# Kernel tuning notes

Measured on AMD Instinct MI355X. Metric: run time of the kernel, lower is better.

Reference implementation:

```python
import jax, jax.numpy as jnp
import numpy as np

B, S, DIN, DOUT = 4, 2048, 4096, 4096

def setup_inputs() -> dict:
    key = jax.random.key(0)
    k1, k2, k3, k4 = jax.random.split(key, 4)
    x = jax.random.normal(k1, (B, S, DIN), dtype=jnp.float32)
    # symmetric int8 weight values in [-127, 127]
    quantized_weight = jax.random.randint(k2, (DOUT, DIN), -127, 128, dtype=jnp.int32).astype(jnp.int8)
    weight_scale = jax.random.uniform(k3, (), dtype=jnp.float32) * 0.01 + 1e-4
    bias = jax.random.normal(k4, (DOUT,), dtype=jnp.float32)
    return {"x": x, "quantized_weight": quantized_weight, "weight_scale": weight_scale, "bias": bias}

def reference(x, quantized_weight, weight_scale, bias) -> jnp.ndarray:
    # dequantize_tensor: (q.float() - 0) * scale
    weight_fp32 = quantized_weight.astype(jnp.float32) * weight_scale  # [DOUT, DIN]
    # nn.functional.linear: x @ W^T + b
    return jnp.einsum('bsi,oi->bso', x, weight_fp32) + bias
```

## Files before the change

### kernel.cpp

```cpp
#include <hip/hip_runtime.h>
#include <stdint.h>
#include <stddef.h>

constexpr int MDIM = 8192;
constexpr int NDIM = 4096;
constexpr int KDIM = 4096;

using f32x4 = __attribute__((ext_vector_type(4))) float;
using s16x4 = __attribute__((ext_vector_type(4))) short;
using i32x4 = __attribute__((ext_vector_type(4))) int;

__device__ __forceinline__ short f32_to_bf16_rn(float f) {
  union { float f; uint32_t u; } v; v.f = f;
  uint32_t r = (v.u + 0x7FFFu + ((v.u >> 16) & 1u)) >> 16;
  return (short)(uint16_t)r;
}

__global__ void __launch_bounds__(256) quant_x_kernel(const float* __restrict__ in,
                                                      signed char* __restrict__ out,
                                                      float* __restrict__ sx) {
  const int row = blockIdx.x;
  const int t   = threadIdx.x;
  const float* rp = in + (size_t)row * KDIM;
  f32x4 v[4];
  float m = 0.0f;
#pragma unroll
  for (int j = 0; j < 4; ++j) {
    v[j] = *(const f32x4*)(rp + t * 16 + j * 4);
#pragma unroll
    for (int e = 0; e < 4; ++e) m = fmaxf(m, __builtin_fabsf(v[j][e]));
  }
#pragma unroll
  for (int off = 32; off > 0; off >>= 1) m = fmaxf(m, __shfl_xor(m, off, 64));
  __shared__ float wmax[4];
  const int wv = t >> 6, ln = t & 63;
  if (ln == 0) wmax[wv] = m;
  __syncthreads();
  m = fmaxf(fmaxf(wmax[0], wmax[1]), fmaxf(wmax[2], wmax[3]));
  const float inv = (m > 0.0f) ? (127.0f / m) : 0.0f;
  if (t == 0) sx[row] = m * (1.0f / 127.0f);
  i32x4 o;
#pragma unroll
  for (int j = 0; j < 4; ++j) {
    int b[4];
#pragma unroll
    for (int e = 0; e < 4; ++e) {
      int q = (int)rintf(v[j][e] * inv);
      q = q < -127 ? -127 : (q > 127 ? 127 : q);
      b[e] = q & 255;
    }
    o[j] = b[0] | (b[1] << 8) | (b[2] << 16) | (b[3] << 24);
  }
  *(i32x4*)(out + (size_t)row * KDIM + t * 16) = o;
}

__global__ void __launch_bounds__(256) quant_w_kernel(const int* __restrict__ in,
                                                      signed char* __restrict__ out, int n16) {
  int i = blockIdx.x * 256 + threadIdx.x;
  const int stride = gridDim.x * 256;
  for (; i < n16; i += stride) {
    const i32x4* p = (const i32x4*)(in + (size_t)i * 16);
    i32x4 o;
#pragma unroll
    for (int j = 0; j < 4; ++j) {
      i32x4 a = p[j];
      o[j] = (a[0] & 255) | ((a[1] & 255) << 8) | ((a[2] & 255) << 16) | ((a[3] & 255) << 24);
    }
    *(i32x4*)(out + (size_t)i * 16) = o;
  }
}


#define BAR asm volatile("s_barrier" ::: "memory")
#define WAITVM6 asm volatile("s_waitcnt vmcnt(6)" ::: "memory")
#define WAITVM0 asm volatile("s_waitcnt vmcnt(0)" ::: "memory")

#define GLL(src, dst) __builtin_amdgcn_global_load_lds(                     \
    (const __attribute__((address_space(1))) void*)(src),                   \
    (__attribute__((address_space(3))) void*)(dst), 16, 0, 0)

#define STAGE(grow, ldsmat, ks, tau) do {                                   \
  const int buf_ = (tau) & 1;                                               \
  GLL((grow) + (size_t)r0 * 4096 + (size_t)(tau) * 128 + (ks) * 64 + cb,    \
      lds + (ldsmat) + buf_ * 32768 + (ks) * 16384 + t * 16);               \
  GLL((grow) + (size_t)r1 * 4096 + (size_t)(tau) * 128 + (ks) * 64 + cb,    \
      lds + (ldsmat) + buf_ * 32768 + (ks) * 16384 + 8192 + t * 16);        \
} while (0)

#define LDA(cur, ks, i) (*(const i32x4*)(lds + (cur) * 32768 + (ks) * 16384 \
    + (wm * 8 + (i)) * 1024 + laneoff))
#define LDB(cur, ks, j) (*(const i32x4*)(lds + 65536 + (cur) * 32768        \
    + (ks) * 16384 + (wn * 4 + (j)) * 1024 + laneoff))

#define READ_B(cur, ks) do {                                                \
  _Pragma("unroll") for (int j = 0; j < 4; ++j) bf[j] = LDB(cur, ks, j);    \
} while (0)
#define READ_A(cur, ks, ibase) do {                                         \
  _Pragma("unroll") for (int i = 0; i < 4; ++i) af[i] = LDA(cur, ks, (ibase) + i); \
} while (0)

#define MFMA16(ibase) do {                                                  \
  __builtin_amdgcn_s_setprio(1);                                            \
  _Pragma("unroll") for (int i = 0; i < 4; ++i)                             \
  _Pragma("unroll") for (int j = 0; j < 4; ++j)                             \
    acc[(ibase) + i][j] = __builtin_amdgcn_mfma_i32_16x16x64_i8(            \
        af[i], bf[j], acc[(ibase) + i][j], 0, 0, 0);                        \
  __builtin_amdgcn_s_setprio(0);                                            \
} while (0)

#define KTILE(t_, cur, nstage, endvm) do {                                  \
                                                   \
  READ_B(cur, 0); READ_A(cur, 0, 0);                                        \
  if ((nstage) >= 1) STAGE(Arow, 0, 1, (t_) + 1);        \
  BAR; MFMA16(0); BAR;                                                      \
                                        \
  READ_A(cur, 0, 4);                                                        \
  if ((nstage) == 4) STAGE(Brow, 65536, 0, (t_) + 2);    \
  BAR; MFMA16(4); BAR;                                                      \
                                                   \
  READ_B(cur, 1); READ_A(cur, 1, 0);                                        \
  if ((nstage) == 4) STAGE(Arow, 0, 0, (t_) + 2);        \
  BAR; MFMA16(0); BAR;                                                      \
                                                   \
  READ_A(cur, 1, 4);                                                        \
  if ((nstage) == 4) STAGE(Brow, 65536, 1, (t_) + 2);    \
  BAR; MFMA16(4);                                                           \
  if ((endvm) == 6) { WAITVM6; } else if ((endvm) == 0) { WAITVM0; }        \
  BAR;                                                                      \
} while (0)

__global__ void __launch_bounds__(512, 2) gemm_i8_8ph(
    const signed char* __restrict__ A, const signed char* __restrict__ Bw,
    const float* __restrict__ sx, const float* __restrict__ scale_p,
    const float* __restrict__ bias, float* __restrict__ out) {
  __shared__ __align__(16) char lds[131072];

  const int t      = threadIdx.x;
  const int lane   = t & 63;
  const int wave   = t >> 6;
  const int wm     = wave >> 2;
  const int wn     = wave & 3;
  const int lane15 = lane & 15;
  const int lh     = lane >> 4;

  const int laneoff = (lane15 * 64 + lh * 16) ^ ((lane15 & 8) << 2);

  const int ax = ((t >> 5) & 1) << 5;
  const int a0 = (t * 16) ^ ax;
  const int a1 = (8192 + t * 16) ^ ax;
  const int r0 = (((a0 >> 10) & 15) << 4) | ((a0 >> 6) & 15);
  const int r1 = (((a1 >> 10) & 15) << 4) | ((a1 >> 6) & 15);
  const int cb = a0 & 63;

  const int bid   = blockIdx.x;
  const int wg    = (bid & 7) * 64 + (bid >> 3);
  const int ntile = wg & 15;
  const int mtile = wg >> 4;
  const int m0 = mtile * 256;
  const int n0 = ntile * 256;

  const char* Arow = (const char*)(A + (size_t)m0 * KDIM);
  const char* Brow = (const char*)(Bw + (size_t)n0 * KDIM);

  i32x4 acc[8][4] = {};
  i32x4 af[4], bf[4];

  STAGE(Brow, 65536, 0, 0);
  STAGE(Arow, 0,     0, 0);
  STAGE(Brow, 65536, 1, 0);
  STAGE(Arow, 0,     1, 0);
  STAGE(Brow, 65536, 0, 1);
  STAGE(Arow, 0,     0, 1);
  STAGE(Brow, 65536, 1, 1);
  WAITVM6;
  BAR;

#pragma unroll 1
  for (int tp = 0; tp < 15; ++tp) {
    const int t2 = tp * 2;
    KTILE(t2,     0, 4, 6);
    KTILE(t2 + 1, 1, 4, 6);
  }
  KTILE(30, 0, 1, 0);
  KTILE(31, 1, 0, -1);

  const float sw = scale_p[0];
  float bv[4];
#pragma unroll
  for (int j = 0; j < 4; ++j) bv[j] = bias[n0 + wn * 64 + j * 16 + lane15];
#pragma unroll
  for (int i = 0; i < 8; ++i) {
    const int rowb = m0 + wm * 128 + i * 16 + lh * 4;
    float sxq[4];
#pragma unroll
    for (int q = 0; q < 4; ++q) sxq[q] = sx[rowb + q] * sw;
#pragma unroll
    for (int j = 0; j < 4; ++j) {
      const int col = n0 + wn * 64 + j * 16 + lane15;
#pragma unroll
      for (int q = 0; q < 4; ++q)
        out[(size_t)(rowb + q) * NDIM + col] = (float)acc[i][j][q] * sxq[q] + bv[j];
    }
  }
}

constexpr int FTILE = 128;
constexpr int FBK   = 64;

__global__ void __launch_bounds__(256) gemm_raw(
    const float* __restrict__ X, const int* __restrict__ W,
    const float* __restrict__ scale_p, const float* __restrict__ bias,
    float* __restrict__ out) {
  __shared__ short As[FTILE * FBK];
  __shared__ short Bs[FTILE * FBK];

  const int t      = threadIdx.x;
  const int lane   = t & 63;
  const int wave   = t >> 6;
  const int wm     = wave >> 1;
  const int wn     = wave & 1;
  const int lane15   = lane & 15;
  const int laneHalf = lane >> 4;

  const int bid   = blockIdx.x;
  const int wg    = (bid & 7) * 256 + (bid >> 3);
  const int ntile = wg & 31;
  const int mtile = wg >> 5;
  const int m0 = mtile * FTILE;
  const int n0 = ntile * FTILE;

  f32x4 acc[4][4] = {};

  for (int k0 = 0; k0 < KDIM; k0 += FBK) {
    __syncthreads();
#pragma unroll
    for (int r = 0; r < 8; ++r) {
      const int f   = r * 256 + t;
      const int row = f >> 4;
      const int c4  = (f & 15) * 4;
      f32x4 v = *(const f32x4*)(X + (size_t)(m0 + row) * KDIM + (k0 + c4));
      s16x4 h;
#pragma unroll
      for (int j = 0; j < 4; ++j) h[j] = f32_to_bf16_rn(v[j]);
      *(s16x4*)&As[row * FBK + c4] = h;

      i32x4 wv = *(const i32x4*)(W + (size_t)(n0 + row) * KDIM + (k0 + c4));
      s16x4 hw;
#pragma unroll
      for (int j = 0; j < 4; ++j) hw[j] = f32_to_bf16_rn((float)wv[j]);
      *(s16x4*)&Bs[row * FBK + c4] = hw;
    }
    __syncthreads();

#pragma unroll
    for (int kk = 0; kk < FBK; kk += 32) {
      const int kb = kk + laneHalf * 8;
      using s16x8f = __attribute__((ext_vector_type(8))) short;
      s16x8f af[4], bf[4];
#pragma unroll
      for (int i = 0; i < 4; ++i) {
        af[i] = *(const s16x8f*)&As[(wm * 64 + i * 16 + lane15) * FBK + kb];
        bf[i] = *(const s16x8f*)&Bs[(wn * 64 + i * 16 + lane15) * FBK + kb];
      }
#pragma unroll
      for (int i = 0; i < 4; ++i)
#pragma unroll
        for (int j = 0; j < 4; ++j)
          acc[i][j] = __builtin_amdgcn_mfma_f32_16x16x32_bf16(af[i], bf[j], acc[i][j], 0, 0, 0);
    }
  }

  const float s = scale_p[0];
#pragma unroll
  for (int j = 0; j < 4; ++j) {
    const int col = n0 + wn * 64 + j * 16 + lane15;
    const float bv = bias[col];
#pragma unroll
    for (int i = 0; i < 4; ++i) {
      const int row = m0 + wm * 64 + i * 16 + laneHalf * 4;
#pragma unroll
      for (int q = 0; q < 4; ++q)
        out[(size_t)(row + q) * NDIM + col] = acc[i][j][q] * s + bv;
    }
  }
}

extern "C" void kernel_launch(void* const* d_in, const int* in_sizes, int n_in,
                              void* d_out, int out_size, void* d_ws, size_t ws_size,
                              hipStream_t stream) {
  const float* x     = (const float*)d_in[0];
  const int*   w     = (const int*)d_in[1];
  const float* scale = (const float*)d_in[2];
  const float* bias  = (const float*)d_in[3];
  float* out = (float*)d_out;

  const size_t a_bytes = (size_t)MDIM * KDIM;
  const size_t b_bytes = (size_t)NDIM * KDIM;
  const size_t need    = a_bytes + b_bytes + MDIM * 4;

  if (ws_size >= need) {
    signed char* Ai8 = (signed char*)d_ws;
    signed char* Bi8 = Ai8 + a_bytes;
    float*       sxp = (float*)(Bi8 + b_bytes);
    quant_x_kernel<<<MDIM, 256, 0, stream>>>(x, Ai8, sxp);
    quant_w_kernel<<<4096, 256, 0, stream>>>(w, Bi8, (int)(b_bytes / 16));
    const int nwg = (MDIM / 256) * (NDIM / 256);
    gemm_i8_8ph<<<nwg, 512, 0, stream>>>(Ai8, Bi8, sxp, scale, bias, out);
  } else {
    const int nwg = (MDIM / FTILE) * (NDIM / FTILE);
    gemm_raw<<<nwg, 256, 0, stream>>>(x, w, scale, bias, out);
  }
}
```

Before: 185.6 us.

## Pre-swizzle quantized activations into MFMA fragment layout and load A directly to registers

```diff
diff --git a/kernel.cpp b/kernel.cpp
--- a/kernel.cpp
+++ b/kernel.cpp
@@ -51,7 +51,10 @@
     }
     o[j] = b[0] | (b[1] << 8) | (b[2] << 16) | (b[3] << 24);
   }
-  *(i32x4*)(out + (size_t)row * KDIM + t * 16) = o;
+  const int fr = row >> 4;
+  const int kc = t >> 2;
+  const int l  = (row & 15) + ((t & 3) << 4);
+  *(i32x4*)(out + (((size_t)(fr * 64 + kc) * 64 + l) << 4)) = o;
 }
 
 __global__ void __launch_bounds__(256) quant_w_kernel(const int* __restrict__ in,
@@ -72,68 +75,71 @@
 
 
 #define BAR asm volatile("s_barrier" ::: "memory")
-#define WAITVM6 asm volatile("s_waitcnt vmcnt(6)" ::: "memory")
-#define WAITVM0 asm volatile("s_waitcnt vmcnt(0)" ::: "memory")
+#define WAITVM(n) asm volatile("s_waitcnt vmcnt(" #n ")" ::: "memory")
 
 #define GLL(src, dst) __builtin_amdgcn_global_load_lds(                     \
     (const __attribute__((address_space(1))) void*)(src),                   \
     (__attribute__((address_space(3))) void*)(dst), 16, 0, 0)
 
-#define STAGE(grow, ldsmat, ks, tau) do {                                   \
+#define STAGEB(ks, tau) do {                                                \
   const int buf_ = (tau) & 1;                                               \
-  GLL((grow) + (size_t)r0 * 4096 + (size_t)(tau) * 128 + (ks) * 64 + cb,    \
-      lds + (ldsmat) + buf_ * 32768 + (ks) * 16384 + t * 16);               \
-  GLL((grow) + (size_t)r1 * 4096 + (size_t)(tau) * 128 + (ks) * 64 + cb,    \
-      lds + (ldsmat) + buf_ * 32768 + (ks) * 16384 + 8192 + t * 16);        \
-} while (0)
-
-#define LDA(cur, ks, i) (*(const i32x4*)(lds + (cur) * 32768 + (ks) * 16384 \
-    + (wm * 8 + (i)) * 1024 + laneoff))
-#define LDB(cur, ks, j) (*(const i32x4*)(lds + 65536 + (cur) * 32768        \
+  GLL(Brow + (size_t)r0 * 4096 + (size_t)(tau) * 128 + (ks) * 64 + cb,      \
+      lds + buf_ * 32768 + (ks) * 16384 + t * 16);                          \
+  GLL(Brow + (size_t)r1 * 4096 + (size_t)(tau) * 128 + (ks) * 64 + cb,      \
+      lds + buf_ * 32768 + (ks) * 16384 + 8192 + t * 16);                   \
+} while (0)
+
+#define LDB(cur, ks, j) (*(const i32x4*)(lds + (cur) * 32768                \
     + (ks) * 16384 + (wn * 4 + (j)) * 1024 + laneoff))
 
 #define READ_B(cur, ks) do {                                                \
   _Pragma("unroll") for (int j = 0; j < 4; ++j) bf[j] = LDB(cur, ks, j);    \
 } while (0)
-#define READ_A(cur, ks, ibase) do {                                         \
-  _Pragma("unroll") for (int i = 0; i < 4; ++i) af[i] = LDA(cur, ks, (ibase) + i); \
-} while (0)
-
-#define MFMA16(ibase) do {                                                  \
+
+#define LDAG(SET, fi0, kc) do {                                             \
+  _Pragma("unroll") for (int i_ = 0; i_ < 4; ++i_)                          \
+    SET[i_] = *(const i32x4*)(ApL                                           \
+        + (((size_t)(frB + (fi0) + i_) * 64 + (kc)) << 10));                \
+} while (0)
+
+#define MFMA16(SET) do {                                                    \
   __builtin_amdgcn_s_setprio(1);                                            \
   _Pragma("unroll") for (int i = 0; i < 4; ++i)                             \
   _Pragma("unroll") for (int j = 0; j < 4; ++j)                             \
-    acc[(ibase) + i][j] = __builtin_amdgcn_mfma_i32_16x16x64_i8(            \
-        af[i], bf[j], acc[(ibase) + i][j], 0, 0, 0);                        \
+    accp[i][j] = __builtin_amdgcn_mfma_i32_16x16x64_i8(                     \
+        SET[i], bf[j], accp[i][j], 0, 0, 0);                                \
   __builtin_amdgcn_s_setprio(0);                                            \
 } while (0)
 
-#define KTILE(t_, cur, nstage, endvm) do {                                  \
-                                                   \
-  READ_B(cur, 0); READ_A(cur, 0, 0);                                        \
-  if ((nstage) >= 1) STAGE(Arow, 0, 1, (t_) + 1);        \
-  BAR; MFMA16(0); BAR;                                                      \
-                                        \
-  READ_A(cur, 0, 4);                                                        \
-  if ((nstage) == 4) STAGE(Brow, 65536, 0, (t_) + 2);    \
-  BAR; MFMA16(4); BAR;                                                      \
-                                                   \
-  READ_B(cur, 1); READ_A(cur, 1, 0);                                        \
-  if ((nstage) == 4) STAGE(Arow, 0, 0, (t_) + 2);        \
-  BAR; MFMA16(0); BAR;                                                      \
-                                                   \
-  READ_A(cur, 1, 4);                                                        \
-  if ((nstage) == 4) STAGE(Brow, 65536, 1, (t_) + 2);    \
-  BAR; MFMA16(4);                                                           \
-  if ((endvm) == 6) { WAITVM6; } else if ((endvm) == 0) { WAITVM0; }        \
+#define MFMA16P do { auto* accp = &acc[0]; MFMA16(afP); } while (0)
+#define MFMA16Q do { auto* accp = &acc[4]; MFMA16(afQ); } while (0)
+
+#define KTILE(t_, cur, nstage, lastA, endvm) do {                           \
+                                                                   \
+  READ_B(cur, 0);                                                           \
+  LDAG(afQ, 4, (t_) * 2 + 0);                                               \
+  if (nstage) STAGEB(0, (t_) + 1);                                          \
+  BAR; MFMA16P; BAR;                                                        \
+                                                       \
+  LDAG(afP, 0, (t_) * 2 + 1);                                               \
+  if (nstage) STAGEB(1, (t_) + 1);                                          \
+  BAR; MFMA16Q; BAR;                                                        \
+                                                                   \
+  READ_B(cur, 1);                                                           \
+  LDAG(afQ, 4, (t_) * 2 + 1);                                               \
+  BAR; MFMA16P; BAR;                                                        \
+                                                                   \
+  if (lastA) LDAG(afP, 0, ((t_) + 1) * 2 + 0);                              \
+  BAR; MFMA16Q;                                                             \
+  if ((endvm) == 8) { WAITVM(8); }                                          \
   BAR;                                                                      \
 } while (0)
 
-__global__ void __launch_bounds__(512, 2) gemm_i8_8ph(
-    const signed char* __restrict__ A, const signed char* __restrict__ Bw,
+__global__ void __launch_bounds__(512, 1) gemm_i8_adir(
+    const signed char* __restrict__ A2, const signed char* __restrict__ Bw,
     const float* __restrict__ sx, const float* __restrict__ scale_p,
     const float* __restrict__ bias, float* __restrict__ out) {
-  __shared__ __align__(16) char lds[131072];
+  __shared__ __align__(16) char lds[65536];
 
   const int t      = threadIdx.x;
   const int lane   = t & 63;
@@ -159,30 +165,26 @@
   const int m0 = mtile * 256;
   const int n0 = ntile * 256;
 
-  const char* Arow = (const char*)(A + (size_t)m0 * KDIM);
   const char* Brow = (const char*)(Bw + (size_t)n0 * KDIM);
+  const signed char* ApL = A2 + lane * 16;
+  const int frB = (m0 >> 4) + wm * 8;
 
   i32x4 acc[8][4] = {};
-  i32x4 af[4], bf[4];
-
-  STAGE(Brow, 65536, 0, 0);
-  STAGE(Arow, 0,     0, 0);
-  STAGE(Brow, 65536, 1, 0);
-  STAGE(Arow, 0,     1, 0);
-  STAGE(Brow, 65536, 0, 1);
-  STAGE(Arow, 0,     0, 1);
-  STAGE(Brow, 65536, 1, 1);
-  WAITVM6;
+  i32x4 afP[4], afQ[4], bf[4];
+
+  STAGEB(0, 0);
+  STAGEB(1, 0);
+  LDAG(afP, 0, 0);
+  WAITVM(0);
   BAR;
 
 #pragma unroll 1
   for (int tp = 0; tp < 15; ++tp) {
-    const int t2 = tp * 2;
-    KTILE(t2,     0, 4, 6);
-    KTILE(t2 + 1, 1, 4, 6);
-  }
-  KTILE(30, 0, 1, 0);
-  KTILE(31, 1, 0, -1);
+    KTILE(2 * tp,     0, 1, 1, 8);
+    KTILE(2 * tp + 1, 1, 1, 1, 8);
+  }
+  KTILE(30, 0, 1, 1, 8);
+  KTILE(31, 1, 0, 0, -1);
 
   const float sw = scale_p[0];
   float bv[4];
@@ -305,7 +307,7 @@
     quant_x_kernel<<<MDIM, 256, 0, stream>>>(x, Ai8, sxp);
     quant_w_kernel<<<4096, 256, 0, stream>>>(w, Bi8, (int)(b_bytes / 16));
     const int nwg = (MDIM / 256) * (NDIM / 256);
-    gemm_i8_8ph<<<nwg, 512, 0, stream>>>(Ai8, Bi8, sxp, scale, bias, out);
+    gemm_i8_adir<<<nwg, 512, 0, stream>>>(Ai8, Bi8, sxp, scale, bias, out);
   } else {
     const int nwg = (MDIM / FTILE) * (NDIM / FTILE);
     gemm_raw<<<nwg, 256, 0, stream>>>(x, w, scale, bias, out);
```

Result: slower. 250.7 us (+35.1%).
